# Kernel tuning notes

Hardware: AMD Instinct MI355X
Metric: run time of the kernel (lower is better)

The kernel has to match this reference:

```python
import jax, jax.numpy as jnp
import numpy as np

B, F0, D = 4096, 39, 16
CROSS_LAYER_SIZE = (128, 128)


def _he_uniform(key, shape):
    fan_in = int(np.prod(shape[:-1]))
    limit = np.sqrt(6.0 / fan_in)
    return jax.random.uniform(key, shape, jnp.float32, -limit, limit)


def setup_inputs() -> dict:
    key = jax.random.key(0)
    k_x, k_f0, k_f1, k_w, k_b = jax.random.split(key, 5)
    x = jax.random.normal(k_x, (B, F0, D), dtype=jnp.float32)
    # field_nums with direct=False: [39, 128//2=64, 64]
    f0 = _he_uniform(k_f0, (F0 * F0, CROSS_LAYER_SIZE[0]))          # (1521, 128)
    f1 = _he_uniform(k_f1, (F0 * (CROSS_LAYER_SIZE[0] // 2), CROSS_LAYER_SIZE[1]))  # (2496, 128)
    out_dim = CROSS_LAYER_SIZE[0] // 2 + CROSS_LAYER_SIZE[1]        # 192
    dense_w = _he_uniform(k_w, (out_dim, 1))
    dense_b = jnp.zeros((1,), dtype=jnp.float32)
    return {"x": x, "f0": f0, "f1": f1, "dense_w": dense_w, "dense_b": dense_b}


def reference(x, f0, f1, dense_w, dense_b):
    # CIN forward (direct=False, use_bias=False, use_residual=False, relu)
    # x: (B, F0, D)
    filters = [f0, f1]
    n_layers = len(CROSS_LAYER_SIZE)
    h = x  # hidden state, (B, Fk, D)
    finals = []
    for idx, L in enumerate(CROSS_LAYER_SIZE):
        Fk = h.shape[1]
        # filter f_ has shape (F0*Fk, L) with i (field of x0) major, j (field of h) minor
        Wr = filters[idx].reshape(F0, Fk, L)
        # fused outer product + conv1d (kernel width 1 == matmul over i,j):
        # z[b, m, d] = sum_{i,j} x[b,i,d] * h[b,j,d] * W[i,j,m]
        z = jnp.einsum('bid,bjd,ijm->bmd', x, h, Wr)  # (B, L, D)
        z = jax.nn.relu(z)
        if idx != n_layers - 1:
            # split along feature-map axis: first half feeds next layer,
            # second half goes to output
            h = z[:, : L // 2, :]
            finals.append(z[:, L // 2:, :])
        else:
            finals.append(z)
    result = jnp.sum(jnp.concatenate(finals, axis=1), axis=-1)  # (B, 192)
    return result @ dense_w + dense_b  # (B, 1)
```

## Files before the change

kernel.cpp:

```cpp
#include <hip/hip_runtime.h>


typedef __attribute__((ext_vector_type(8)))  short bf16x8;
typedef __attribute__((ext_vector_type(16))) float f32x16;

static __device__ __forceinline__ unsigned short f2bf_rne(float f) {
    unsigned int u = __builtin_bit_cast(unsigned int, f);
    u = (u + 0x7FFFu + ((u >> 16) & 1u)) >> 16;
    return (unsigned short)u;
}
static __device__ __forceinline__ unsigned int pk_trunc(float a, float b) {
    unsigned int ua = __builtin_bit_cast(unsigned int, a);
    unsigned int ub = __builtin_bit_cast(unsigned int, b);
    return (ua >> 16) | (ub & 0xffff0000u);
}

__global__ __launch_bounds__(256)
void CIN_repack(const float* __restrict__ f0, const float* __restrict__ f1,
                unsigned int* __restrict__ ws)
{
    const int tid  = blockIdx.x * 256 + threadIdx.x;
    const int tp   = tid & 3;
    const int lane = (tid >> 2) & 63;
    const int cg   = (tid >> 8) & 3;
    const int kh   = (tid >> 10) & 1;
    const int ch   = tid >> 11;
    const int half = lane >> 5;
    const int n    = cg * 32 + (lane & 31);
    const int t0   = tp * 2;
    float v0, v1;
    if (ch < 50) {
        const int ig = ch / 5, jg = ch - ig * 5;
        const int i = ig * 4 + kh * 2 + half;
        const int j = jg * 8 + t0;
        const bool iok = (i < 39);
        v0 = (iok && j     < 39) ? f0[(i * 39 + j    ) * 128 + n] : 0.f;
        v1 = (iok && j + 1 < 39) ? f0[(i * 39 + j + 1) * 128 + n] : 0.f;
    } else {
        const int c1 = ch - 50;
        const int jg = c1 / 5, ig = c1 - jg * 5;
        const int j = jg * 4 + kh * 2 + half;
        const int i = ig * 8 + t0;
        v0 = (i     < 39) ? f1[( i      * 64 + j) * 128 + n] : 0.f;
        v1 = (i + 1 < 39) ? f1[((i + 1) * 64 + j) * 128 + n] : 0.f;
    }
    ws[tid] = (unsigned int)f2bf_rne(v0) | ((unsigned int)f2bf_rne(v1) << 16);
}

static __device__ __forceinline__ bf16x8 build8(float xi, float4 a, float4 b) {
    union { unsigned int u[4]; bf16x8 v; } r;
    r.u[0] = pk_trunc(xi * a.x, xi * a.y);
    r.u[1] = pk_trunc(xi * a.z, xi * a.w);
    r.u[2] = pk_trunc(xi * b.x, xi * b.y);
    r.u[3] = pk_trunc(xi * b.z, xi * b.w);
    return r.v;
}

__global__ __launch_bounds__(256, 2)
void CIN_main(const float* __restrict__ x,
              const char* __restrict__ wsB,
              const float* __restrict__ dw,
              const float* __restrict__ db,
              float* __restrict__ out)
{
    __shared__ __align__(16) float xsTi[8][40][16];
    __shared__ __align__(16) float xsTd[8][16][44];
    __shared__ __align__(16) float hsT[8][64][17];
    __shared__ float dws[192];
    __shared__ float red[2][2][4];

    const int tid  = threadIdx.x;
    const int w    = tid >> 6;
    const int lane = tid & 63;
    const int g    = w & 1;
    const int hh   = w >> 1;
    const int half = lane >> 5;
    const int d    = lane & 15;
    const int bsel = (lane >> 4) & 1;
    const int g4   = g * 4;

    const float4* xg4 = (const float4*)(x + (size_t)blockIdx.x * 8 * 624);
    for (int e4 = tid; e4 < 1248; e4 += 256) {
        float4 v = xg4[e4];
        int bb = e4 / 156, r = e4 - bb * 156;
        int i = r >> 2, d0 = (r & 3) * 4;
        *(float4*)&xsTi[bb][i][d0] = v;
        xsTd[bb][d0 + 0][i] = v.x; xsTd[bb][d0 + 1][i] = v.y;
        xsTd[bb][d0 + 2][i] = v.z; xsTd[bb][d0 + 3][i] = v.w;
    }
    if (tid < 128) { int bb = tid >> 4, dd = tid & 15; xsTi[bb][39][dd] = 0.f; xsTd[bb][dd][39] = 0.f; }
    if (tid < 192) dws[tid] = dw[tid];
    __syncthreads();

    float4 xv[2][10];
#pragma unroll
    for (int p = 0; p < 2; ++p) {
        const float* src = &xsTd[g4 + p * 2 + bsel][d][0];
#pragma unroll
        for (int q = 0; q < 10; ++q) xv[p][q] = *(const float4*)(src + q * 4);
    }

    const char* wlane = wsB + lane * 16;
    bf16x8 Bc[2][2], Bn[2][2];
    auto loadB = [&](int ch, bf16x8 (&B)[2][2]) {
        const char* base = wlane + (size_t)ch * 8192;
#pragma unroll
        for (int kh = 0; kh < 2; ++kh)
#pragma unroll
            for (int c = 0; c < 2; ++c)
                B[kh][c] = *(const bf16x8*)(base + kh * 4096 + (hh * 2 + c) * 1024);
    };

    f32x16 acc[2][2];
#pragma unroll
    for (int p = 0; p < 2; ++p)
#pragma unroll
        for (int c = 0; c < 2; ++c)
#pragma unroll
            for (int r = 0; r < 16; ++r) acc[p][c][r] = 0.f;

    loadB(0, Bc);

    for (int ig = 0; ig < 10; ++ig) {
        float xiv[2][2];
#pragma unroll
        for (int p = 0; p < 2; ++p)
#pragma unroll
            for (int kh = 0; kh < 2; ++kh)
                xiv[p][kh] = xsTi[g4 + p * 2 + bsel][ig * 4 + kh * 2 + half][d];
#pragma unroll
        for (int jg = 0; jg < 5; ++jg) {
            const int ch = ig * 5 + jg;
            loadB(ch + 1, Bn);
            bf16x8 A[2][2];
#pragma unroll
            for (int p = 0; p < 2; ++p)
#pragma unroll
                for (int kh = 0; kh < 2; ++kh)
                    A[p][kh] = build8(xiv[p][kh], xv[p][jg * 2], xv[p][jg * 2 + 1]);
#pragma unroll
            for (int p = 0; p < 2; ++p)
#pragma unroll
                for (int c = 0; c < 2; ++c) {
                    acc[p][c] = __builtin_amdgcn_mfma_f32_32x32x16_bf16(A[p][0], Bc[0][c], acc[p][c], 0, 0, 0);
                    acc[p][c] = __builtin_amdgcn_mfma_f32_32x32x16_bf16(A[p][1], Bc[1][c], acc[p][c], 0, 0, 0);
                }
#pragma unroll
            for (int kh = 0; kh < 2; ++kh)
#pragma unroll
                for (int c = 0; c < 2; ++c) Bc[kh][c] = Bn[kh][c];
        }
    }

    float cs[4] = {0.f, 0.f, 0.f, 0.f};
    if (hh == 0) {
#pragma unroll
        for (int p = 0; p < 2; ++p)
#pragma unroll
            for (int c = 0; c < 2; ++c)
#pragma unroll
                for (int r = 0; r < 16; ++r) {
                    const int row = (r & 3) + 8 * (r >> 2) + 4 * half;
                    hsT[g4 + p * 2 + (row >> 4)][c * 32 + (lane & 31)][row & 15] =
                        fmaxf(acc[p][c][r], 0.f);
                }
    } else {
#pragma unroll
        for (int p = 0; p < 2; ++p)
#pragma unroll
            for (int c = 0; c < 2; ++c) {
                const float dwv = dws[c * 32 + (lane & 31)];
#pragma unroll
                for (int r = 0; r < 16; ++r) {
                    const int row = (r & 3) + 8 * (r >> 2) + 4 * half;
                    cs[p * 2 + (row >> 4)] += fmaxf(acc[p][c][r], 0.f) * dwv;
                }
            }
    }
#pragma unroll
    for (int p = 0; p < 2; ++p)
#pragma unroll
        for (int c = 0; c < 2; ++c)
#pragma unroll
            for (int r = 0; r < 16; ++r) acc[p][c][r] = 0.f;
    __syncthreads();

    for (int jg = 0; jg < 16; ++jg) {
        float hjv[2][2];
#pragma unroll
        for (int p = 0; p < 2; ++p)
#pragma unroll
            for (int kh = 0; kh < 2; ++kh)
                hjv[p][kh] = hsT[g4 + p * 2 + bsel][jg * 4 + kh * 2 + half][d];
#pragma unroll
        for (int ig2 = 0; ig2 < 5; ++ig2) {
            const int ch = 50 + jg * 5 + ig2;
            const int chn = (ch < 129) ? ch + 1 : 129;
            loadB(chn, Bn);
            bf16x8 A[2][2];
#pragma unroll
            for (int p = 0; p < 2; ++p)
#pragma unroll
                for (int kh = 0; kh < 2; ++kh)
                    A[p][kh] = build8(hjv[p][kh], xv[p][ig2 * 2], xv[p][ig2 * 2 + 1]);
#pragma unroll
            for (int p = 0; p < 2; ++p)
#pragma unroll
                for (int c = 0; c < 2; ++c) {
                    acc[p][c] = __builtin_amdgcn_mfma_f32_32x32x16_bf16(A[p][0], Bc[0][c], acc[p][c], 0, 0, 0);
                    acc[p][c] = __builtin_amdgcn_mfma_f32_32x32x16_bf16(A[p][1], Bc[1][c], acc[p][c], 0, 0, 0);
                }
#pragma unroll
            for (int kh = 0; kh < 2; ++kh)
#pragma unroll
                for (int c = 0; c < 2; ++c) Bc[kh][c] = Bn[kh][c];
        }
    }

#pragma unroll
    for (int p = 0; p < 2; ++p)
#pragma unroll
        for (int c = 0; c < 2; ++c) {
            const float dwv = dws[64 + (2 * hh + c) * 32 + (lane & 31)];
#pragma unroll
            for (int r = 0; r < 16; ++r) {
                const int row = (r & 3) + 8 * (r >> 2) + 4 * half;
                cs[p * 2 + (row >> 4)] += fmaxf(acc[p][c][r], 0.f) * dwv;
            }
        }
#pragma unroll
    for (int rr = 0; rr < 4; ++rr)
#pragma unroll
        for (int off = 32; off > 0; off >>= 1)
            cs[rr] += __shfl_xor(cs[rr], off, 64);
    if (lane == 0) {
#pragma unroll
        for (int rr = 0; rr < 4; ++rr) red[g][hh][rr] = cs[rr];
    }
    __syncthreads();
    if (tid < 8) {
        const int g2 = tid >> 2, rr = tid & 3;
        out[blockIdx.x * 8 + g2 * 4 + rr] = red[g2][0][rr] + red[g2][1][rr] + db[0];
    }
}

extern "C" void kernel_launch(void* const* d_in, const int* in_sizes, int n_in,
                              void* d_out, int out_size, void* d_ws, size_t ws_size,
                              hipStream_t stream)
{
    const float* x  = (const float*)d_in[0];
    const float* f0 = (const float*)d_in[1];
    const float* f1 = (const float*)d_in[2];
    const float* dw = (const float*)d_in[3];
    const float* db = (const float*)d_in[4];
    float* out = (float*)d_out;

    CIN_repack<<<dim3(1040), dim3(256), 0, stream>>>(f0, f1, (unsigned int*)d_ws);
    CIN_main<<<dim3(512), dim3(256), 0, stream>>>(x, (const char*)d_ws, dw, db, out);
}
```

Measured before the change: 129.7 us.

## Stage bf16 filter chunks into LDS with async global_load_lds double buffering

Instead of every wave prefetching its own filter fragments from global memory into registers, each 8 KB weight chunk is loaded once per block straight into a double-buffered LDS area with global_load_lds. The MFMA B operands are then read from LDS. A block-wide barrier after each chunk keeps the two buffers in order. The repack kernel now has threads read consecutive filter columns and scatter to the packed layout, and the separate i-major x copy in LDS is dropped in favour of reads from the d-major copy. The aim is to cut redundant global/L2 weight traffic and register pressure, at the cost of one barrier per chunk (130 per block) and extra LDS traffic.

```diff
diff --git a/kernel.cpp b/kernel.cpp
--- a/kernel.cpp
+++ b/kernel.cpp
@@ -20,13 +20,12 @@
                 unsigned int* __restrict__ ws)
 {
     const int tid  = blockIdx.x * 256 + threadIdx.x;
-    const int tp   = tid & 3;
-    const int lane = (tid >> 2) & 63;
-    const int cg   = (tid >> 8) & 3;
-    const int kh   = (tid >> 10) & 1;
-    const int ch   = tid >> 11;
-    const int half = lane >> 5;
-    const int n    = cg * 32 + (lane & 31);
+    const int n    = tid & 127;
+    const int slot = tid >> 7;
+    const int tp   = slot & 3;
+    const int half = (slot >> 2) & 1;
+    const int kh   = (slot >> 3) & 1;
+    const int ch   = slot >> 4;
     const int t0   = tp * 2;
     float v0, v1;
     if (ch < 50) {
@@ -44,7 +43,10 @@
         v0 = (i     < 39) ? f1[( i      * 64 + j) * 128 + n] : 0.f;
         v1 = (i + 1 < 39) ? f1[((i + 1) * 64 + j) * 128 + n] : 0.f;
     }
-    ws[tid] = (unsigned int)f2bf_rne(v0) | ((unsigned int)f2bf_rne(v1) << 16);
+    const int lane = half * 32 + (n & 31);
+    const int cg   = n >> 5;
+    const int dst  = ch * 2048 + kh * 1024 + cg * 256 + lane * 4 + tp;
+    ws[dst] = (unsigned int)f2bf_rne(v0) | ((unsigned int)f2bf_rne(v1) << 16);
 }
 
 static __device__ __forceinline__ bf16x8 build8(float xi, float4 a, float4 b) {
@@ -63,7 +65,7 @@
               const float* __restrict__ db,
               float* __restrict__ out)
 {
-    __shared__ __align__(16) float xsTi[8][40][16];
+    __shared__ __align__(16) unsigned short Bsh[2][4096];
     __shared__ __align__(16) float xsTd[8][16][44];
     __shared__ __align__(16) float hsT[8][64][17];
     __shared__ float dws[192];
@@ -79,16 +81,36 @@
     const int bsel = (lane >> 4) & 1;
     const int g4   = g * 4;
 
+    auto stage = [&](int ch) {
+        const char* src = wsB + (size_t)ch * 8192 + w * 2048 + lane * 16;
+        unsigned short* dst = &Bsh[ch & 1][w * 1024];
+        __builtin_amdgcn_global_load_lds(
+            (const __attribute__((address_space(1))) void*)src,
+            (__attribute__((address_space(3))) void*)dst, 16, 0, 0);
+        __builtin_amdgcn_global_load_lds(
+            (const __attribute__((address_space(1))) void*)(src + 1024),
+            (__attribute__((address_space(3))) void*)(dst + 512), 16, 0, 0);
+    };
+    auto loadB = [&](int ch, bf16x8 (&B)[2][2]) {
+        const char* base = (const char*)&Bsh[ch & 1][0] + lane * 16;
+#pragma unroll
+        for (int kh = 0; kh < 2; ++kh)
+#pragma unroll
+            for (int c = 0; c < 2; ++c)
+                B[kh][c] = *(const bf16x8*)(base + kh * 4096 + (hh * 2 + c) * 1024);
+    };
+
+    stage(0);
+
     const float4* xg4 = (const float4*)(x + (size_t)blockIdx.x * 8 * 624);
     for (int e4 = tid; e4 < 1248; e4 += 256) {
         float4 v = xg4[e4];
         int bb = e4 / 156, r = e4 - bb * 156;
         int i = r >> 2, d0 = (r & 3) * 4;
-        *(float4*)&xsTi[bb][i][d0] = v;
         xsTd[bb][d0 + 0][i] = v.x; xsTd[bb][d0 + 1][i] = v.y;
         xsTd[bb][d0 + 2][i] = v.z; xsTd[bb][d0 + 3][i] = v.w;
     }
-    if (tid < 128) { int bb = tid >> 4, dd = tid & 15; xsTi[bb][39][dd] = 0.f; xsTd[bb][dd][39] = 0.f; }
+    if (tid < 128) { int bb = tid >> 4, dd = tid & 15; xsTd[bb][dd][39] = 0.f; }
     if (tid < 192) dws[tid] = dw[tid];
     __syncthreads();
 
@@ -100,17 +122,6 @@
         for (int q = 0; q < 10; ++q) xv[p][q] = *(const float4*)(src + q * 4);
     }
 
-    const char* wlane = wsB + lane * 16;
-    bf16x8 Bc[2][2], Bn[2][2];
-    auto loadB = [&](int ch, bf16x8 (&B)[2][2]) {
-        const char* base = wlane + (size_t)ch * 8192;
-#pragma unroll
-        for (int kh = 0; kh < 2; ++kh)
-#pragma unroll
-            for (int c = 0; c < 2; ++c)
-                B[kh][c] = *(const bf16x8*)(base + kh * 4096 + (hh * 2 + c) * 1024);
-    };
-
     f32x16 acc[2][2];
 #pragma unroll
     for (int p = 0; p < 2; ++p)
@@ -118,8 +129,6 @@
         for (int c = 0; c < 2; ++c)
 #pragma unroll
             for (int r = 0; r < 16; ++r) acc[p][c][r] = 0.f;
-
-    loadB(0, Bc);
 
     for (int ig = 0; ig < 10; ++ig) {
         float xiv[2][2];
@@ -127,11 +136,13 @@
         for (int p = 0; p < 2; ++p)
 #pragma unroll
             for (int kh = 0; kh < 2; ++kh)
-                xiv[p][kh] = xsTi[g4 + p * 2 + bsel][ig * 4 + kh * 2 + half][d];
+                xiv[p][kh] = xsTd[g4 + p * 2 + bsel][d][ig * 4 + kh * 2 + half];
 #pragma unroll
         for (int jg = 0; jg < 5; ++jg) {
             const int ch = ig * 5 + jg;
-            loadB(ch + 1, Bn);
+            stage(ch + 1);
+            bf16x8 Bf[2][2];
+            loadB(ch, Bf);
             bf16x8 A[2][2];
 #pragma unroll
             for (int p = 0; p < 2; ++p)
@@ -142,13 +153,10 @@
             for (int p = 0; p < 2; ++p)
 #pragma unroll
                 for (int c = 0; c < 2; ++c) {
-                    acc[p][c] = __builtin_amdgcn_mfma_f32_32x32x16_bf16(A[p][0], Bc[0][c], acc[p][c], 0, 0, 0);
-                    acc[p][c] = __builtin_amdgcn_mfma_f32_32x32x16_bf16(A[p][1], Bc[1][c], acc[p][c], 0, 0, 0);
-                }
-#pragma unroll
-            for (int kh = 0; kh < 2; ++kh)
-#pragma unroll
-                for (int c = 0; c < 2; ++c) Bc[kh][c] = Bn[kh][c];
+                    acc[p][c] = __builtin_amdgcn_mfma_f32_32x32x16_bf16(A[p][0], Bf[0][c], acc[p][c], 0, 0, 0);
+                    acc[p][c] = __builtin_amdgcn_mfma_f32_32x32x16_bf16(A[p][1], Bf[1][c], acc[p][c], 0, 0, 0);
+                }
+            __syncthreads();
         }
     }
 
@@ -195,8 +203,9 @@
 #pragma unroll
         for (int ig2 = 0; ig2 < 5; ++ig2) {
             const int ch = 50 + jg * 5 + ig2;
-            const int chn = (ch < 129) ? ch + 1 : 129;
-            loadB(chn, Bn);
+            if (ch < 129) stage(ch + 1);
+            bf16x8 Bf[2][2];
+            loadB(ch, Bf);
             bf16x8 A[2][2];
 #pragma unroll
             for (int p = 0; p < 2; ++p)
@@ -207,13 +216,10 @@
             for (int p = 0; p < 2; ++p)
 #pragma unroll
                 for (int c = 0; c < 2; ++c) {
-                    acc[p][c] = __builtin_amdgcn_mfma_f32_32x32x16_bf16(A[p][0], Bc[0][c], acc[p][c], 0, 0, 0);
-                    acc[p][c] = __builtin_amdgcn_mfma_f32_32x32x16_bf16(A[p][1], Bc[1][c], acc[p][c], 0, 0, 0);
-                }
-#pragma unroll
-            for (int kh = 0; kh < 2; ++kh)
-#pragma unroll
-                for (int c = 0; c < 2; ++c) Bc[kh][c] = Bn[kh][c];
+                    acc[p][c] = __builtin_amdgcn_mfma_f32_32x32x16_bf16(A[p][0], Bf[0][c], acc[p][c], 0, 0, 0);
+                    acc[p][c] = __builtin_amdgcn_mfma_f32_32x32x16_bf16(A[p][1], Bf[1][c], acc[p][c], 0, 0, 0);
+                }
+            __syncthreads();
         }
     }
 
```

New measurement: 137.4 us. 6.0% more time.
